# Optimization experiments

Measured on AMD Instinct MI355X. Metric: run time of the kernel, lower is better.

Reference implementation:

```python
import jax, jax.numpy as jnp
import numpy as np

N_HEADS = 16
B = 8
SEQ = 1024
HID = 1024
TOT = B * SEQ


def setup_inputs() -> dict:
    key = jax.random.key(0)
    k1, k2, k3 = jax.random.split(key, 3)
    hidden_states = jax.random.normal(k1, (TOT, HID), dtype=jnp.float32)
    Wqkv = jax.random.normal(k2, (3 * HID, HID), dtype=jnp.float32) * 0.02
    Bqkv = jax.random.normal(k3, (3 * HID,), dtype=jnp.float32) * 0.02
    cu_seqlens = (jnp.arange(B + 1, dtype=jnp.int32) * SEQ)
    return {"hidden_states": hidden_states, "Wqkv": Wqkv, "Bqkv": Bqkv,
            "cu_seqlens": cu_seqlens, "max_s": SEQ}


def reference(hidden_states, Wqkv, Bqkv, cu_seqlens, max_s):
    # qkv projection: F.linear(hidden, Wqkv, Bqkv) -> [T, 3H]
    T, H = hidden_states.shape
    h = N_HEADS
    d = H // h
    b = cu_seqlens.shape[0] - 1
    S = T // b  # equal-length packing; cu_seqlens = arange(b+1)*S
    qkv = hidden_states @ Wqkv.T + Bqkv                      # [T, 3H]
    qkv = qkv.reshape(b, S, 3, h, d)
    q, k, v = qkv[:, :, 0], qkv[:, :, 1], qkv[:, :, 2]       # [b, S, h, d]
    scale = 1.0 / jnp.sqrt(jnp.asarray(d, dtype=q.dtype))
    scores = jnp.einsum("bshd,bthd->bhst", q, k) * scale     # [b, h, S, S]
    probs = jax.nn.softmax(scores, axis=-1)                  # p_dropout = 0.0
    ctx = jnp.einsum("bhst,bthd->bshd", probs, v)            # [b, S, h, d]
    return ctx.reshape(T, H)
```

## Files before the change

### kernel.cpp

```cpp
#include <hip/hip_runtime.h>

typedef __attribute__((ext_vector_type(8))) __bf16 bf16x8;
typedef __attribute__((ext_vector_type(2))) __bf16 bf16x2;
typedef __attribute__((ext_vector_type(4))) float f32x4;
typedef __attribute__((ext_vector_type(4))) unsigned int u32x4;

#define AS1 __attribute__((address_space(1)))
#define AS3 __attribute__((address_space(3)))

__device__ __forceinline__ unsigned short f2b(float f) {
    union { float f; unsigned int u; } c; c.f = f;
    unsigned int r = c.u + 0x7fffu + ((c.u >> 16) & 1u);
    return (unsigned short)(r >> 16);
}

__device__ __forceinline__ unsigned int pack2(float a, float b) {
    bf16x2 t;
    t[0] = (__bf16)a;
    t[1] = (__bf16)b;
    return __builtin_bit_cast(unsigned int, t);
}

__device__ __forceinline__ void gload_lds16(const void* g, void* l) {
    __builtin_amdgcn_global_load_lds((const AS1 unsigned int*)g,
                                     (AS3 unsigned int*)l, 16, 0, 0);
}

__global__ void cvt2_kernel(const float* __restrict__ in0,
                            unsigned short* __restrict__ out0, int n0,
                            const float* __restrict__ in1,
                            unsigned short* __restrict__ out1, int n1) {
    int i = blockIdx.x * blockDim.x + threadIdx.x;
    int stride = gridDim.x * blockDim.x;
    const int nt = n0 + n1;
    for (; i < nt; i += stride) {
        if (i < n0) {
            float4 v = reinterpret_cast<const float4*>(in0)[i];
            ushort4 o;
            o.x = f2b(v.x); o.y = f2b(v.y); o.z = f2b(v.z); o.w = f2b(v.w);
            reinterpret_cast<ushort4*>(out0)[i] = o;
        } else {
            const int j = i - n0;
            float4 v = reinterpret_cast<const float4*>(in1)[j];
            ushort4 o;
            o.x = f2b(v.x); o.y = f2b(v.y); o.z = f2b(v.z); o.w = f2b(v.w);
            reinterpret_cast<ushort4*>(out1)[j] = o;
        }
    }
}

__global__ __launch_bounds__(512, 4) void qkv_gemm(
    const unsigned short* __restrict__ A,
    const unsigned short* __restrict__ Bw,
    const float* __restrict__ bias,
    unsigned short* __restrict__ qb,
    unsigned short* __restrict__ kb,
    unsigned short* __restrict__ vb)
{
    __shared__ __align__(16) char smem[73728];
    const int tid = threadIdx.x;
    const int lane = tid & 63, w = tid >> 6;
    const int wm = w >> 1, wn = w & 1;
    const int wg = (blockIdx.x & 7) * 96 + (blockIdx.x >> 3);
    const int mt = wg / 24;
    const int nt = wg % 24;
    const int fr = lane & 15, kg = lane >> 4;

    const int sr = lane >> 2;
    const int g  = (lane & 3) ^ ((sr >> 1) & 3);
    const unsigned short* a_srcg = A  + (size_t)(mt * 256 + w * 16 + sr) * 1024 + g * 8;
    const unsigned short* b_srcg = Bw + (size_t)(nt * 128 + w * 16 + sr) * 1024 + g * 8;

    f32x4 acc[4][4] = {};
    const int pg = (kg ^ ((fr >> 1) & 3)) * 16;
    const int aoffA = (wm * 64 + fr) * 64;
    const int boffB = (wn * 64 + fr) * 64;

#define STAGE_FULL(buf, kt) do {                                    \
    char* Sb_ = smem + (buf) * 24576 + w * 1024;                    \
    const size_t ko_ = (size_t)(kt) * 32;                           \
    gload_lds16(a_srcg + ko_,          Sb_);                        \
    gload_lds16(a_srcg + 131072 + ko_, Sb_ + 8192);                 \
    gload_lds16(b_srcg + ko_,          Sb_ + 16384);                \
} while (0)

#define MM(m_, n_) do {                                                        \
    acc[m_][n_] = __builtin_amdgcn_mfma_f32_16x16x32_bf16(                     \
        af[m_], bf[n_], acc[m_][n_], 0, 0, 0);                                 \
} while (0)

#define GT1(CUR, PRE, kt, DOSTAGE, WNSTR) do {                                 \
    const char* Ab_ = smem + (CUR) * 24576;                                    \
    const char* Bb_ = Ab_ + 16384;                                             \
    char* Sb_ = smem + (PRE) * 24576 + w * 1024;                               \
    const size_t ko_ = (size_t)((kt) + 2) * 32;                                \
    bf16x8 af[4], bf[4];                                                       \
    _Pragma("unroll")                                                          \
    for (int n = 0; n < 4; ++n)                                                \
        bf[n] = *reinterpret_cast<const bf16x8*>(Bb_ + boffB + n * 1024 + pg); \
    _Pragma("unroll")                                                          \
    for (int m = 0; m < 4; ++m)                                                \
        af[m] = *reinterpret_cast<const bf16x8*>(Ab_ + aoffA + m * 1024 + pg); \
    if (DOSTAGE) {                                                             \
        gload_lds16(a_srcg + ko_,          Sb_);                               \
        gload_lds16(a_srcg + 131072 + ko_, Sb_ + 8192);                        \
        gload_lds16(b_srcg + ko_,          Sb_ + 16384);                       \
    }                                                                          \
    asm volatile("s_waitcnt vmcnt(" WNSTR ")" ::: "memory");                   \
    __builtin_amdgcn_s_barrier();                                              \
    __builtin_amdgcn_s_setprio(1);                                             \
    MM(0, 0); MM(0, 1); MM(0, 2); MM(0, 3);                                    \
    MM(1, 0); MM(1, 1); MM(1, 2); MM(1, 3);                                    \
    MM(2, 0); MM(2, 1); MM(2, 2); MM(2, 3);                                    \
    MM(3, 0); MM(3, 1); MM(3, 2); MM(3, 3);                                    \
    __builtin_amdgcn_s_setprio(0);                                             \
    __builtin_amdgcn_s_barrier();                                              \
} while (0)

    STAGE_FULL(0, 0);
    STAGE_FULL(1, 1);
    asm volatile("s_waitcnt vmcnt(3)" ::: "memory");
    __builtin_amdgcn_s_barrier();
#pragma unroll 1
    for (int it = 0; it < 10; ++it) {
        const int t0 = it * 3;
        GT1(0, 2, t0 + 0, 1, "3");
        GT1(1, 0, t0 + 1, 1, "3");
        GT1(2, 1, t0 + 2, 1, "3");
    }
    GT1(0, 2, 30, 0, "0");
    GT1(1, 0, 31, 0, "0");
    __syncthreads();

    const int sidx = nt >> 3;
    float bv[4];
#pragma unroll
    for (int n = 0; n < 4; ++n) bv[n] = bias[nt * 128 + wn * 64 + n * 16 + fr];

    unsigned short* Cs = (unsigned short*)smem;

    if (sidx < 2) {
        unsigned short* dstb = (sidx == 0) ? qb : kb;
        const float sc = (sidx == 0) ? 0.1803368801111f : 1.0f;
#pragma unroll
        for (int p = 0; p < 2; ++p) {
            if ((wm >> 1) == p) {
                const int r0 = (wm & 1) * 64;
#pragma unroll
                for (int m = 0; m < 4; ++m)
#pragma unroll
                    for (int n = 0; n < 4; ++n)
#pragma unroll
                        for (int r = 0; r < 4; ++r)
                            Cs[(r0 + m * 16 + kg * 4 + r) * 136 + wn * 64 + n * 16 + fr] =
                                f2b((acc[m][n][r] + bv[n]) * sc);
            }
            __syncthreads();
#pragma unroll
            for (int itc = 0; itc < 4; ++itc) {
                const int task = itc * 512 + tid;
                const int rl = task >> 4;
                const int i16 = task & 15;
                const int t = mt * 256 + p * 128 + rl;
                const int b_ = t >> 10, s = t & 1023;
                const int head = ((nt * 128 + i16 * 8) >> 6) & 15;
                u32x4 v = *reinterpret_cast<const u32x4*>(Cs + rl * 136 + i16 * 8);
                *reinterpret_cast<u32x4*>(
                    dstb + ((size_t)(b_ * 16 + head) * 1024 + s) * 64 + (i16 & 7) * 8) = v;
            }
            __syncthreads();
        }
    } else {
#pragma unroll
        for (int p = 0; p < 2; ++p) {
            if ((wm >> 1) == p) {
                const int r0 = (wm & 1) * 64;
#pragma unroll
                for (int m = 0; m < 4; ++m)
#pragma unroll
                    for (int n = 0; n < 4; ++n)
#pragma unroll
                        for (int j = 0; j < 2; ++j) {
                            unsigned int pk = pack2(acc[m][n][2 * j] + bv[n],
                                                    acc[m][n][2 * j + 1] + bv[n]);
                            *reinterpret_cast<unsigned int*>(
                                Cs + (wn * 64 + n * 16 + fr) * 136
                                   + r0 + m * 16 + kg * 4 + 2 * j) = pk;
                        }
            }
            __syncthreads();
#pragma unroll
            for (int itc = 0; itc < 4; ++itc) {
                const int task = itc * 512 + tid;
                const int c = task >> 4;
                const int i16 = task & 15;
                const int col = nt * 128 + c;
                const int head = (col >> 6) & 15;
                const int d = col & 63;
                const int b_ = (mt * 256) >> 10;
                const int s0 = (mt * 256 & 1023) + p * 128 + i16 * 8;
                u32x4 v = *reinterpret_cast<const u32x4*>(Cs + c * 136 + i16 * 8);
                *reinterpret_cast<u32x4*>(
                    vb + (size_t)((b_ * 16 + head) * 64 + d) * 1024 + s0) = v;
            }
            __syncthreads();
        }
    }
#undef STAGE_FULL
#undef GT1
#undef MM
}

#define KVB 64
__global__ __launch_bounds__(256, 4) void attn_kernel(
    const unsigned short* __restrict__ qb,
    const unsigned short* __restrict__ kb,
    const unsigned short* __restrict__ vb,
    float* __restrict__ out)
{
    __shared__ __align__(16) char asmem[32768];
    const int tid = threadIdx.x;
    const int lane = tid & 63, w = tid >> 6;
    const int wg = (blockIdx.x & 7) * 128 + (blockIdx.x >> 3);
    const int bh = wg >> 3;
    const int qt = wg & 7;
    const int b_ = bh >> 4, h_ = bh & 15;
    const int fr = lane & 15, kg = lane >> 4;

    const unsigned short* qp = qb + ((size_t)bh * 1024 + qt * 128) * 64;
    const unsigned short* kp = kb + (size_t)bh * 1024 * 64;
    const unsigned short* vp = vb + (size_t)bh * 64 * 1024;

    bf16x8 qfr[2][2];
#pragma unroll
    for (int qf = 0; qf < 2; ++qf) {
        const unsigned short* qr = qp + (w * 32 + qf * 16 + fr) * 64 + kg * 8;
        qfr[qf][0] = *reinterpret_cast<const bf16x8*>(qr);
        qfr[qf][1] = *reinterpret_cast<const bf16x8*>(qr + 32);
    }

    float m_q[2] = {-1e30f, -1e30f}, l_q[2] = {0.f, 0.f};
    f32x4 o_acc[2][4] = {};

    const int ksr = w * 8 + (lane >> 3);
    const int kcb = (lane & 7) * 16;

#define ASTAGE(buf, kvt) do {                                                  \
    const int kv0_ = (kvt) * KVB;                                              \
    char* Kb_ = asmem + (buf) * 16384 + w * 1024;                              \
    char* Vb_ = Kb_ + 8192;                                                    \
    _Pragma("unroll")                                                          \
    for (int i = 0; i < 2; ++i) {                                              \
        const int st = i * 32 + ksr;                                           \
        const int key = ((st >> 5) << 5) | (((st & 15) >> 2) << 3)             \
                      | (((st >> 4) & 1) << 2) | (st & 3);                     \
        const int scb = kcb ^ ((st & 7) << 4);                                 \
        gload_lds16(kp + (size_t)(kv0_ + key) * 64 + (scb >> 1),               \
                    Kb_ + i * 4096);                                           \
        const int d_ = i * 32 + ksr;                                           \
        const int svb = kcb ^ ((d_ & 7) << 4);                                 \
        gload_lds16(vp + (size_t)d_ * 1024 + kv0_ + (svb >> 1),                \
                    Vb_ + i * 4096);                                           \
    }                                                                          \
} while (0)

#define ACOMP(buf) do {                                                        \
    const char* Kb = asmem + (buf) * 16384;                                    \
    const char* Vb = Kb + 8192;                                                \
    f32x4 sacc[2][4] = {};                                                     \
    __builtin_amdgcn_s_setprio(1);                                             \
    _Pragma("unroll")                                                          \
    for (int jt = 0; jt < 4; ++jt) {                                           \
        _Pragma("unroll")                                                      \
        for (int ks = 0; ks < 2; ++ks) {                                       \
            const int cb = (ks * 64 + kg * 16) ^ ((fr & 7) << 4);              \
            bf16x8 kf = *reinterpret_cast<const bf16x8*>(                      \
                Kb + (jt * 16 + fr) * 128 + cb);                               \
            _Pragma("unroll")                                                  \
            for (int qf = 0; qf < 2; ++qf)                                     \
                sacc[qf][jt] = __builtin_amdgcn_mfma_f32_16x16x32_bf16(        \
                    kf, qfr[qf][ks], sacc[qf][jt], 0, 0, 0);                   \
        }                                                                      \
    }                                                                          \
    __builtin_amdgcn_s_setprio(0);                                             \
    unsigned int P2[2][4][2];                                                  \
    _Pragma("unroll")                                                          \
    for (int qf = 0; qf < 2; ++qf) {                                           \
        float mx = -1e30f;                                                     \
        _Pragma("unroll")                                                      \
        for (int jt = 0; jt < 4; ++jt) {                                       \
            float a = fmaxf(fmaxf(sacc[qf][jt][0], sacc[qf][jt][1]),           \
                            fmaxf(sacc[qf][jt][2], sacc[qf][jt][3]));          \
            mx = fmaxf(mx, a);                                                 \
        }                                                                      \
        mx = fmaxf(mx, __shfl_xor(mx, 16, 64));                                \
        mx = fmaxf(mx, __shfl_xor(mx, 32, 64));                                \
        if (__any(mx > m_q[qf] + 8.0f)) {                                      \
            const float mn = fmaxf(m_q[qf], mx);                               \
            const float corr = __builtin_amdgcn_exp2f(m_q[qf] - mn);           \
            m_q[qf] = mn;                                                      \
            l_q[qf] *= corr;                                                   \
            float cr[4];                                                       \
            _Pragma("unroll")                                                  \
            for (int r = 0; r < 4; ++r)                                        \
                cr[r] = __shfl(corr, kg * 4 + r, 64);                          \
            _Pragma("unroll")                                                  \
            for (int d0 = 0; d0 < 4; ++d0)                                     \
                _Pragma("unroll")                                              \
                for (int r = 0; r < 4; ++r) o_acc[qf][d0][r] *= cr[r];         \
        }                                                                      \
        const float mn_ = m_q[qf];                                             \
        float rs = 0.f;                                                        \
        _Pragma("unroll")                                                      \
        for (int jt = 0; jt < 4; ++jt) {                                       \
            float p0 = __builtin_amdgcn_exp2f(sacc[qf][jt][0] - mn_);          \
            float p1 = __builtin_amdgcn_exp2f(sacc[qf][jt][1] - mn_);          \
            float p2 = __builtin_amdgcn_exp2f(sacc[qf][jt][2] - mn_);          \
            float p3 = __builtin_amdgcn_exp2f(sacc[qf][jt][3] - mn_);          \
            rs += (p0 + p1) + (p2 + p3);                                       \
            P2[qf][jt][0] = pack2(p0, p1);                                     \
            P2[qf][jt][1] = pack2(p2, p3);                                     \
        }                                                                      \
        rs += __shfl_xor(rs, 16, 64);                                          \
        rs += __shfl_xor(rs, 32, 64);                                          \
        l_q[qf] += rs;                                                         \
    }                                                                          \
    __builtin_amdgcn_s_setprio(1);                                             \
    _Pragma("unroll")                                                          \
    for (int c = 0; c < 2; ++c) {                                              \
        bf16x8 pa[2];                                                          \
        _Pragma("unroll")                                                      \
        for (int qf = 0; qf < 2; ++qf) {                                       \
            u32x4 pw = { P2[qf][2 * c][0], P2[qf][2 * c][1],                   \
                         P2[qf][2 * c + 1][0], P2[qf][2 * c + 1][1] };         \
            pa[qf] = __builtin_bit_cast(bf16x8, pw);                           \
        }                                                                      \
        _Pragma("unroll")                                                      \
        for (int d0 = 0; d0 < 4; ++d0) {                                       \
            const int dd = d0 * 16 + fr;                                       \
            const int cbv = (c * 64 + kg * 16) ^ ((dd & 7) << 4);              \
            bf16x8 vf = *reinterpret_cast<const bf16x8*>(Vb + dd * 128 + cbv); \
            _Pragma("unroll")                                                  \
            for (int qf = 0; qf < 2; ++qf)                                     \
                o_acc[qf][d0] = __builtin_amdgcn_mfma_f32_16x16x32_bf16(       \
                    pa[qf], vf, o_acc[qf][d0], 0, 0, 0);                       \
        }                                                                      \
    }                                                                          \
    __builtin_amdgcn_s_setprio(0);                                             \
} while (0)

    ASTAGE(0, 0);
#pragma unroll 1
    for (int t = 0; t < 15; ++t) {
        ASTAGE((t + 1) & 1, t + 1);
        asm volatile("s_waitcnt vmcnt(4) lgkmcnt(0)" ::: "memory");
        __builtin_amdgcn_s_barrier();
        ACOMP(t & 1);
        asm volatile("s_waitcnt lgkmcnt(0)" ::: "memory");
        __builtin_amdgcn_s_barrier();
    }
    asm volatile("s_waitcnt vmcnt(0) lgkmcnt(0)" ::: "memory");
    __builtin_amdgcn_s_barrier();
    ACOMP(1);

#pragma unroll
    for (int qf = 0; qf < 2; ++qf) {
        float linv[4];
#pragma unroll
        for (int r = 0; r < 4; ++r)
            linv[r] = 1.0f / __shfl(l_q[qf], kg * 4 + r, 64);
        const int trow = b_ * 1024 + qt * 128 + w * 32 + qf * 16;
#pragma unroll
        for (int d0 = 0; d0 < 4; ++d0) {
            const int c = h_ * 64 + d0 * 16 + fr;
#pragma unroll
            for (int r = 0; r < 4; ++r)
                out[(size_t)(trow + kg * 4 + r) * 1024 + c] = o_acc[qf][d0][r] * linv[r];
        }
    }
#undef ASTAGE
#undef ACOMP
}

extern "C" void kernel_launch(void* const* d_in, const int* in_sizes, int n_in,
                              void* d_out, int out_size, void* d_ws, size_t ws_size,
                              hipStream_t stream)
{
    const float* hs   = (const float*)d_in[0];
    const float* Wqkv = (const float*)d_in[1];
    const float* Bqkv = (const float*)d_in[2];
    float* out = (float*)d_out;

    char* ws = (char*)d_ws;
    unsigned short* hsb = (unsigned short*)(ws);
    unsigned short* wb  = (unsigned short*)(ws + (size_t)16 * 1048576);
    unsigned short* qb  = (unsigned short*)(ws + (size_t)22 * 1048576);
    unsigned short* kb  = (unsigned short*)(ws + (size_t)38 * 1048576);
    unsigned short* vb  = (unsigned short*)(ws + (size_t)54 * 1048576);

    cvt2_kernel<<<2048, 256, 0, stream>>>(hs, hsb, 8192 * 1024 / 4,
                                          Wqkv, wb, 3072 * 1024 / 4);
    qkv_gemm<<<768, 512, 0, stream>>>(hsb, wb, Bqkv, qb, kb, vb);
    attn_kernel<<<1024, 256, 0, stream>>>(qb, kb, vb, out);
}
```

Before: 127.4 us.

## Pre-swizzle weight into MFMA fragment layout and load B directly from global

The weight conversion kernel now writes Wqkv in a fragment-major layout that matches the MFMA operand order. The GEMM can then load B fragments straight from global memory into registers, with no LDS staging. This cuts LDS usage from 72KB to 48KB per block, removes one of the two barriers per k-step, and reorders the MFMA issue to iterate over m first. In exchange, B reads go through the cache hierarchy with less latency hiding, and the hand-set vmcnt wait counts must still cover both the direct B loads and the async A stages.

Result: slower. 147.7 us (+15.9%).

```diff
diff --git a/kernel.cpp b/kernel.cpp
--- a/kernel.cpp
+++ b/kernel.cpp
@@ -41,10 +41,17 @@
             reinterpret_cast<ushort4*>(out0)[i] = o;
         } else {
             const int j = i - n0;
+            const int E = j * 4;
+            const int row = E >> 10;
+            const int col = E & 1023;
             float4 v = reinterpret_cast<const float4*>(in1)[j];
             ushort4 o;
             o.x = f2b(v.x); o.y = f2b(v.y); o.z = f2b(v.z); o.w = f2b(v.w);
-            reinterpret_cast<ushort4*>(out1)[j] = o;
+            const int kt = col >> 5, kg = (col >> 3) & 3, e = col & 7;
+            const int n16 = row >> 4, fr = row & 15;
+            const size_t oaddr = ((size_t)(kt * 192 + n16) << 9)
+                               + ((kg * 16 + fr) << 3) + e;
+            *reinterpret_cast<ushort4*>(out1 + oaddr) = o;
         }
     }
 }
@@ -57,7 +64,7 @@
     unsigned short* __restrict__ kb,
     unsigned short* __restrict__ vb)
 {
-    __shared__ __align__(16) char smem[73728];
+    __shared__ __align__(16) char smem[49152];
     const int tid = threadIdx.x;
     const int lane = tid & 63, w = tid >> 6;
     const int wm = w >> 1, wn = w & 1;
@@ -68,20 +75,18 @@
 
     const int sr = lane >> 2;
     const int g  = (lane & 3) ^ ((sr >> 1) & 3);
-    const unsigned short* a_srcg = A  + (size_t)(mt * 256 + w * 16 + sr) * 1024 + g * 8;
-    const unsigned short* b_srcg = Bw + (size_t)(nt * 128 + w * 16 + sr) * 1024 + g * 8;
+    const unsigned short* a_srcg = A + (size_t)(mt * 256 + w * 16 + sr) * 1024 + g * 8;
+    const unsigned short* bfp = Bw + (((size_t)(nt * 8 + wn * 4)) << 9) + lane * 8;
 
     f32x4 acc[4][4] = {};
     const int pg = (kg ^ ((fr >> 1) & 3)) * 16;
     const int aoffA = (wm * 64 + fr) * 64;
-    const int boffB = (wn * 64 + fr) * 64;
 
 #define STAGE_FULL(buf, kt) do {                                    \
-    char* Sb_ = smem + (buf) * 24576 + w * 1024;                    \
+    char* Sb_ = smem + (buf) * 16384 + w * 1024;                    \
     const size_t ko_ = (size_t)(kt) * 32;                           \
     gload_lds16(a_srcg + ko_,          Sb_);                        \
     gload_lds16(a_srcg + 131072 + ko_, Sb_ + 8192);                 \
-    gload_lds16(b_srcg + ko_,          Sb_ + 16384);                \
 } while (0)
 
 #define MM(m_, n_) do {                                                        \
@@ -89,47 +94,43 @@
         af[m_], bf[n_], acc[m_][n_], 0, 0, 0);                                 \
 } while (0)
 
-#define GT1(CUR, PRE, kt, DOSTAGE, WNSTR) do {                                 \
-    const char* Ab_ = smem + (CUR) * 24576;                                    \
-    const char* Bb_ = Ab_ + 16384;                                             \
-    char* Sb_ = smem + (PRE) * 24576 + w * 1024;                               \
+#define GT(CUR, PRE, kt, DOSTAGE, WNSTR) do {                                  \
+    const char* Ab_ = smem + (CUR) * 16384;                                    \
+    char* Sb_ = smem + (PRE) * 16384 + w * 1024;                               \
     const size_t ko_ = (size_t)((kt) + 2) * 32;                                \
+    const unsigned short* bq_ = bfp + (size_t)(kt) * 98304;                    \
     bf16x8 af[4], bf[4];                                                       \
     _Pragma("unroll")                                                          \
     for (int n = 0; n < 4; ++n)                                                \
-        bf[n] = *reinterpret_cast<const bf16x8*>(Bb_ + boffB + n * 1024 + pg); \
+        bf[n] = *reinterpret_cast<const bf16x8*>(bq_ + (n << 9));              \
+    asm volatile("s_waitcnt vmcnt(" WNSTR ")" ::: "memory");                   \
+    __builtin_amdgcn_s_barrier();                                              \
     _Pragma("unroll")                                                          \
     for (int m = 0; m < 4; ++m)                                                \
         af[m] = *reinterpret_cast<const bf16x8*>(Ab_ + aoffA + m * 1024 + pg); \
     if (DOSTAGE) {                                                             \
         gload_lds16(a_srcg + ko_,          Sb_);                               \
         gload_lds16(a_srcg + 131072 + ko_, Sb_ + 8192);                        \
-        gload_lds16(b_srcg + ko_,          Sb_ + 16384);                       \
     }                                                                          \
-    asm volatile("s_waitcnt vmcnt(" WNSTR ")" ::: "memory");                   \
-    __builtin_amdgcn_s_barrier();                                              \
     __builtin_amdgcn_s_setprio(1);                                             \
-    MM(0, 0); MM(0, 1); MM(0, 2); MM(0, 3);                                    \
-    MM(1, 0); MM(1, 1); MM(1, 2); MM(1, 3);                                    \
-    MM(2, 0); MM(2, 1); MM(2, 2); MM(2, 3);                                    \
-    MM(3, 0); MM(3, 1); MM(3, 2); MM(3, 3);                                    \
+    MM(0, 0); MM(1, 0); MM(2, 0); MM(3, 0);                                    \
+    MM(0, 1); MM(1, 1); MM(2, 1); MM(3, 1);                                    \
+    MM(0, 2); MM(1, 2); MM(2, 2); MM(3, 2);                                    \
+    MM(0, 3); MM(1, 3); MM(2, 3); MM(3, 3);                                    \
     __builtin_amdgcn_s_setprio(0);                                             \
-    __builtin_amdgcn_s_barrier();                                              \
 } while (0)
 
     STAGE_FULL(0, 0);
     STAGE_FULL(1, 1);
-    asm volatile("s_waitcnt vmcnt(3)" ::: "memory");
-    __builtin_amdgcn_s_barrier();
 #pragma unroll 1
     for (int it = 0; it < 10; ++it) {
         const int t0 = it * 3;
-        GT1(0, 2, t0 + 0, 1, "3");
-        GT1(1, 0, t0 + 1, 1, "3");
-        GT1(2, 1, t0 + 2, 1, "3");
-    }
-    GT1(0, 2, 30, 0, "0");
-    GT1(1, 0, 31, 0, "0");
+        GT(0, 2, t0 + 0, 1, "6");
+        GT(1, 0, t0 + 1, 1, "6");
+        GT(2, 1, t0 + 2, 1, "6");
+    }
+    GT(0, 2, 30, 0, "6");
+    GT(1, 0, 31, 0, "4");
     __syncthreads();
 
     const int sidx = nt >> 3;
@@ -207,7 +208,7 @@
         }
     }
 #undef STAGE_FULL
-#undef GT1
+#undef GT
 #undef MM
 }
 
```
